# Kernel tuning notes

Measured on AMD Instinct MI355X. Metric: run time of the kernel, lower is better.

The kernel has to match this reference:

```python
import jax, jax.numpy as jnp
import numpy as np
from jax import lax

Z_DIM = 64
ZS_SIZE = [[1, 1]] * 12 + [[2, 1]] + [[2, 2]] * 11 + [[4, 2]] + [[4, 4]] * 11  # 36 embeddings
FILTER = [[16, 16]] * 6 + [[16, 32]] + [[32, 32]] * 5 + [[32, 64]] + [[64, 64]] * 5  # 18 blocks
OFFS = np.cumsum([0] + [h * k for h, k in ZS_SIZE]).tolist()  # 242 z-vectors total


def _hyper(Z, hn_w2, hn_b2, hn_w1, hn_b1):
    # Batched HyperNetwork: Z [n, 64] -> kernels [n, 16, 16, 3, 3]
    n = Z.shape[0]
    h_in = (Z @ hn_w2 + hn_b2).reshape(n, 16, Z_DIM)            # [n, 16, 64]
    h_fin = jnp.einsum('nid,do->nio', h_in, hn_w1) + hn_b1       # [n, 16, 144]
    return h_fin.reshape(n, 16, 16, 3, 3)


def _make_w(z_all, idx, hn_w2, hn_b2, hn_w1, hn_b1):
    # Assemble conv weight [h*16, k*16, 3, 3] from h*k hypernet tiles (cat dim=1 over k, dim=0 over h)
    h, k = ZS_SIZE[idx]
    Z = z_all[OFFS[idx]:OFFS[idx] + h * k]
    K = _hyper(Z, hn_w2, hn_b2, hn_w1, hn_b1)                    # [h*k, 16, 16, 3, 3]
    K = K.reshape(h, k, 16, 16, 3, 3).transpose(0, 2, 1, 3, 4, 5)
    return K.reshape(h * 16, k * 16, 3, 3)


def _conv(x, w, stride, pad):
    return lax.conv_general_dilated(x, w, (stride, stride), [(pad, pad), (pad, pad)],
                                    dimension_numbers=('NCHW', 'OIHW', 'NCHW'))


def _bn(x, i, g, b, m, v):
    # eval-mode BatchNorm2d with running stats; params padded to 64 channels
    C = x.shape[1]
    gg = g[i, :C].reshape(1, C, 1, 1)
    bb = b[i, :C].reshape(1, C, 1, 1)
    mm = m[i, :C].reshape(1, C, 1, 1)
    vv = v[i, :C].reshape(1, C, 1, 1)
    return (x - mm) * (gg * lax.rsqrt(vv + 1e-5)) + bb


def setup_inputs() -> dict:
    key = jax.random.key(0)
    ks = jax.random.split(key, 16)
    B = 1024
    x = jax.random.normal(ks[0], (B, 3, 32, 32), jnp.float32)
    conv1_w = jax.random.normal(ks[1], (16, 3, 3, 3), jnp.float32) / np.float32(np.sqrt(27.0))
    conv1_b = jnp.zeros((16,), jnp.float32)
    n_bn = 37  # bn1 + 2 per block
    bn_gamma = jnp.ones((n_bn, 64), jnp.float32)
    bn_beta = jnp.zeros((n_bn, 64), jnp.float32)
    bn_mean = jnp.zeros((n_bn, 64), jnp.float32)
    bn_var = jnp.ones((n_bn, 64), jnp.float32)
    hn_w2 = jax.random.normal(ks[2], (Z_DIM, 16 * Z_DIM), jnp.float32) * 0.04
    hn_b2 = jax.random.normal(ks[3], (16 * Z_DIM,), jnp.float32) * 0.01
    hn_w1 = jax.random.normal(ks[4], (Z_DIM, 16 * 9), jnp.float32) * 0.04
    hn_b1 = jax.random.normal(ks[5], (16 * 9,), jnp.float32) * 0.01
    z_all = jax.random.normal(ks[6], (OFFS[-1], Z_DIM), jnp.float32)
    res_w6 = jax.random.normal(ks[7], (32, 16, 1, 1), jnp.float32) * 0.25
    res_b6 = jnp.zeros((32,), jnp.float32)
    res_w12 = jax.random.normal(ks[8], (64, 32, 1, 1), jnp.float32) * 0.18
    res_b12 = jnp.zeros((64,), jnp.float32)
    fin_w = jax.random.normal(ks[9], (10, 64), jnp.float32) * 0.1
    fin_b = jnp.zeros((10,), jnp.float32)
    return {"x": x, "conv1_w": conv1_w, "conv1_b": conv1_b,
            "bn_gamma": bn_gamma, "bn_beta": bn_beta, "bn_mean": bn_mean, "bn_var": bn_var,
            "hn_w2": hn_w2, "hn_b2": hn_b2, "hn_w1": hn_w1, "hn_b1": hn_b1,
            "z_all": z_all, "res_w6": res_w6, "res_b6": res_b6,
            "res_w12": res_w12, "res_b12": res_b12, "fin_w": fin_w, "fin_b": fin_b}


def reference(x, conv1_w, conv1_b, bn_gamma, bn_beta, bn_mean, bn_var,
              hn_w2, hn_b2, hn_w1, hn_b1, z_all,
              res_w6, res_b6, res_w12, res_b12, fin_w, fin_b):
    x = _conv(x, conv1_w, 1, 1) + conv1_b.reshape(1, -1, 1, 1)
    x = jax.nn.relu(_bn(x, 0, bn_gamma, bn_beta, bn_mean, bn_var))
    for i in range(18):
        w1 = _make_w(z_all, 2 * i, hn_w2, hn_b2, hn_w1, hn_b1)
        w2 = _make_w(z_all, 2 * i + 1, hn_w2, hn_b2, hn_w1, hn_b1)
        down = (i > 5 and i % 6 == 0)
        if down:
            rw, rb = (res_w6, res_b6) if i == 6 else (res_w12, res_b12)
            res = _conv(x, rw, 2, 0) + rb.reshape(1, -1, 1, 1)
            stride = 2
        else:
            res = x
            stride = 1
        out = jax.nn.relu(_bn(_conv(x, w1, stride, 1), 1 + 2 * i, bn_gamma, bn_beta, bn_mean, bn_var))
        out = _bn(_conv(out, w2, 1, 1), 2 + 2 * i, bn_gamma, bn_beta, bn_mean, bn_var)
        x = jax.nn.relu(out + res)
    x = x.mean(axis=(2, 3))  # AvgPool2d(8) on [B,64,8,8]
    return x @ fin_w.T + fin_b
```

## Files before the change

### kernel.cpp

```cpp
#include <hip/hip_runtime.h>
#include <hip/hip_bf16.h>


typedef __attribute__((ext_vector_type(8))) short bf16x8;
typedef __attribute__((ext_vector_type(4))) float f32x4;
typedef __attribute__((ext_vector_type(16))) float f32x16;
typedef unsigned short ushort_t;

#define OFFS_LIST {0,1,2,3,4,5,6,7,8,9,10,11,12,14,18,22,26,30,34,38,42,46,50,54,58,66,82,98,114,130,146,162,178,194,210,226,242}
#define K_LIST    {1,1,1,1,1,1,1,1,1,1,1,1,1,2,2,2,2,2,2,2,2,2,2,2,2,4,4,4,4,4,4,4,4,4,4,4}
#define H_LIST    {1,1,1,1,1,1,1,1,1,1,1,1,2,2,2,2,2,2,2,2,2,2,2,2,4,4,4,4,4,4,4,4,4,4,4,4}
#define WOFF_LIST {0,2304,4608,6912,9216,11520,13824,16128,18432,20736,23040,25344,27648,32256,41472,50688,59904,69120,78336,87552,96768,105984,115200,124416,133632,152064,188928,225792,262656,299520,336384,373248,410112,446976,483840,520704}
#define CIN_LIST  {16,16,16,16,16,16,16,16,16,16,16,16,16,32,32,32,32,32,32,32,32,32,32,32,32,64,64,64,64,64,64,64,64,64,64,64}
#define COUT_LIST {16,16,16,16,16,16,16,16,16,16,16,16,32,32,32,32,32,32,32,32,32,32,32,32,64,64,64,64,64,64,64,64,64,64,64,64}
#define WFOFF_LIST {0,7680,15360,23040,30720,38400,46080,53760,61440,69120,76800,84480,92160,107520,135168,165888,196608,227328,258048,288768,319488,350208,380928,411648,442368,503808,632832,755712,878592,1001472,1124352,1247232,1370112,1492992,1615872,1738752}

__constant__ int d_offs[37]  = OFFS_LIST;
__constant__ int d_k[36]     = K_LIST;
__constant__ int d_hh[36]    = H_LIST;
__constant__ int d_woff[36]  = WOFF_LIST;
__constant__ int d_cin[36]   = CIN_LIST;
__constant__ int d_cout[36]  = COUT_LIST;
__constant__ int d_wfoff[36] = WFOFF_LIST;

__device__ inline void split3(float x, ushort_t& h, ushort_t& m, ushort_t& l) {
    unsigned xb = __float_as_uint(x);
    unsigned hb = (xb + 0x8000u) >> 16;
    float fh = __uint_as_float(hb << 16);
    float r = x - fh;
    unsigned mb = (__float_as_uint(r) + 0x8000u) >> 16;
    float fm = __uint_as_float(mb << 16);
    float r2 = r - fm;
    unsigned lb = (__float_as_uint(r2) + 0x8000u) >> 16;
    h = (ushort_t)hb; m = (ushort_t)mb; l = (ushort_t)lb;
}

__global__ void prep(const float* __restrict__ g, const float* __restrict__ be,
                     const float* __restrict__ m, const float* __restrict__ v,
                     const float* __restrict__ rw6, const float* __restrict__ rb12,
                     float* __restrict__ sc, float* __restrict__ sh,
                     float* __restrict__ rwT6, float* __restrict__ shp25) {
    int i = blockIdx.x * blockDim.x + threadIdx.x;
    if (i < 2368) {
        float s = g[i] * rsqrtf(v[i] + 1e-5f);
        sc[i] = s;
        sh[i] = be[i] - m[i] * s;
    } else if (i < 2368 + 512) {
        int t = i - 2368;
        int co = t % 32, ci = t / 32;
        rwT6[ci * 32 + co] = rw6[co * 16 + ci];
    } else if (i < 2368 + 512 + 64) {
        int c = i - 2880;
        int idx2 = 26 * 64 + c;
        float s = g[idx2] * rsqrtf(v[idx2] + 1e-5f);
        shp25[c] = be[idx2] - m[idx2] * s + rb12[c];
    }
}

__global__ void hyper_kernel(const float* __restrict__ z_all, const float* __restrict__ w2,
                             const float* __restrict__ b2, const float* __restrict__ w1,
                             const float* __restrict__ b1, const float* __restrict__ bnsc,
                             float* __restrict__ Wg) {
    int n = blockIdx.x;
    int tid = threadIdx.x;
    __shared__ float zrow[64];
    __shared__ float hin[1024];
    if (tid < 64) zrow[tid] = z_all[n * 64 + tid];
    __syncthreads();
    for (int mcol = tid; mcol < 1024; mcol += 256) {
        float acc = b2[mcol];
        #pragma unroll 8
        for (int d = 0; d < 64; ++d) acc += zrow[d] * w2[d * 1024 + mcol];
        hin[mcol] = acc;
    }
    __syncthreads();
    int L = 0;
    while (n >= d_offs[L + 1]) ++L;
    int r = n - d_offs[L];
    int kk = d_k[L];
    int a = r / kk, bb = r % kk;
    int Cin = kk * 16;
    int Cout = d_hh[L] * 16;
    const float* scp = bnsc + (L + 1) * 64;
    float* wp = Wg + d_woff[L];
    for (int e = tid; e < 2304; e += 256) {
        int i = e / 144, o = e % 144;
        int j = o / 9, tap = o % 9;
        float acc = b1[o];
        #pragma unroll 8
        for (int d = 0; d < 64; ++d) acc += hin[i * 64 + d] * w1[d * 144 + o];
        int co = a * 16 + i;
        acc *= scp[co];
        wp[(tap * Cin + (bb * 16 + j)) * Cout + co] = acc;
    }
}

__global__ void split_w(const float* __restrict__ Wg, const float* __restrict__ rw12,
                        ushort_t* __restrict__ Wf) {
    int L = blockIdx.y;
    int CIN = d_cin[L], COUT = d_cout[L];
    int idx = blockIdx.x * 256 + threadIdx.x;
    int j = idx & 7, lane = (idx >> 3) & 63, t = idx >> 9;
    int hi = lane >> 5;
    float wv;
    int base;
    if (L < 14) {
        int K = 9 * CIN, NKS = (K + 31) / 32, NT = COUT / 16;
        if (t >= NKS * NT) return;
        int nt = t % NT, ks = t / NT;
        int k = ks * 32 + (lane >> 4) * 8 + j;
        int co = nt * 16 + (lane & 15);
        wv = (k < K) ? Wg[d_woff[L] + k * COUT + co] : 0.f;
        base = d_wfoff[L] + ((ks * NT + nt) * 3) * 512 + lane * 8 + j;
    } else {
        int CG8 = CIN / 8, NKS = 5 * CG8, NT = COUT / 32;
        int TKS = NKS + ((L == 25) ? 2 : 0);
        if (t >= TKS * NT) return;
        int nt = t % NT, ks = t / NT;
        int co = nt * 32 + (lane & 31);
        if (ks < NKS) {
            int o = 2 * ks + hi, tap = o % 10, c8 = o / 10;
            int ci = c8 * 8 + j;
            wv = (tap < 9) ? Wg[d_woff[L] + (tap * CIN + ci) * COUT + co] : 0.f;
        } else {
            int k = (ks - NKS) * 16 + hi * 8 + j;
            wv = rw12[co * 32 + k];
        }
        base = d_wfoff[L] + ((ks * NT + nt) * 3) * 512 + lane * 8 + j;
    }
    ushort_t h, m, l;
    split3(wv, h, m, l);
    Wf[base] = h; Wf[base + 512] = m; Wf[base + 1024] = l;
}

__global__ void conv_first(const float* __restrict__ x, const float* __restrict__ cw,
                           const float* __restrict__ cb, const float* __restrict__ g,
                           const float* __restrict__ be, const float* __restrict__ m,
                           const float* __restrict__ v, float* __restrict__ out) {
    int idx = blockIdx.x * 256 + threadIdx.x;
    int px = idx & 31; int t = idx >> 5;
    int py = t & 31;   int b = t >> 5;
    float acc[16];
    #pragma unroll
    for (int co = 0; co < 16; ++co) acc[co] = 0.f;
    const float* ip = x + (long)b * 3 * 1024;
    #pragma unroll 1
    for (int ci = 0; ci < 3; ++ci) {
        #pragma unroll 1
        for (int ky = 0; ky < 3; ++ky) {
            int iy = py + ky - 1;
            if ((unsigned)iy >= 32u) continue;
            #pragma unroll
            for (int kx = 0; kx < 3; ++kx) {
                int ix = px + kx - 1;
                if ((unsigned)ix < 32u) {
                    float xv = ip[ci * 1024 + iy * 32 + ix];
                    #pragma unroll
                    for (int co = 0; co < 16; ++co)
                        acc[co] += xv * cw[co * 27 + ci * 9 + ky * 3 + kx];
                }
            }
        }
    }
    long o = ((long)(b * 32 + py) * 32 + px) * 16;
    #pragma unroll
    for (int co = 0; co < 16; ++co) {
        float s = g[co] * rsqrtf(v[co] + 1e-5f);
        float val = (acc[co] + cb[co] - m[co]) * s + be[co];
        out[o + co] = fmaxf(val, 0.f);
    }
}

__global__ void pad_zero_f32(float* __restrict__ buf, int H2, int C4) {
    int idx = blockIdx.x * 256 + threadIdx.x;
    int nb = 2 * H2 + 2 * (H2 - 2);
    int total = 1024 * nb * C4;
    if (idx >= total) return;
    int ch = idx % C4; int t = idx / C4;
    int bp = t % nb; int img = t / nb;
    int y, x;
    if (bp < H2) { y = 0; x = bp; }
    else if (bp < 2 * H2) { y = H2 - 1; x = bp - H2; }
    else { int s = bp - 2 * H2; y = 1 + (s >> 1); x = (s & 1) ? H2 - 1 : 0; }
    long off = (((long)img * H2 + y) * H2 + x) * (C4 * 4) + ch * 4;
    *(float4*)(buf + off) = make_float4(0.f, 0.f, 0.f, 0.f);
}

template<int MODE>
__global__ __launch_bounds__(256) void conv_s1(
        const float* __restrict__ in, const ushort_t* __restrict__ wf,
        const float* __restrict__ shp, const float* __restrict__ res,
        float* __restrict__ out) {
    constexpr int W2 = 34, SLABPIX = 10 * W2;
    constexpr int NKS = 5;

    __shared__ uint4 lds[6 * SLABPIX];

    int tid = threadIdx.x, lane = tid & 63, wid = tid >> 6;
    int g = lane >> 4, r16 = lane & 15;
    int bid = blockIdx.x;
    int img = bid >> 2, blocky = bid & 3;
    int row0 = blocky * 8;

    const ushort_t* wfl = wf + lane * 8;
    bf16x8 wv[NKS][3];
    #pragma unroll
    for (int ks = 0; ks < NKS; ++ks)
        #pragma unroll
        for (int p = 0; p < 3; ++p)
            wv[ks][p] = *(const bf16x8*)(wfl + (ks * 3 + p) * 512);
    #pragma unroll
    for (int ks = 0; ks < NKS; ++ks)
        #pragma unroll
        for (int p = 0; p < 3; ++p)
            asm volatile("" : "+v"(wv[ks][p]));

    const float* ib = in + (long)img * (32 * 32 * 16);
    for (int it = tid; it < SLABPIX * 2; it += 256) {
        int pix = it % SLABPIX, cc = it / SLABPIX;
        int sr = pix / W2, sc = pix % W2;
        int gy = row0 - 1 + sr, gx = sc - 1;
        float vv[8];
        if ((unsigned)gy < 32u && (unsigned)gx < 32u) {
            const float4* p4 = (const float4*)(ib + ((long)gy * 32 + gx) * 16 + cc * 8);
            float4 a0 = p4[0], a1 = p4[1];
            vv[0]=a0.x; vv[1]=a0.y; vv[2]=a0.z; vv[3]=a0.w;
            vv[4]=a1.x; vv[5]=a1.y; vv[6]=a1.z; vv[7]=a1.w;
        } else {
            #pragma unroll
            for (int q = 0; q < 8; ++q) vv[q] = 0.f;
        }
        union { ushort_t u[8]; uint4 q; } H, M, L;
        #pragma unroll
        for (int q = 0; q < 8; ++q) split3(vv[q], H.u[q], M.u[q], L.u[q]);
        lds[(cc * 3 + 0) * SLABPIX + pix] = H.q;
        lds[(cc * 3 + 1) * SLABPIX + pix] = M.q;
        lds[(cc * 3 + 2) * SLABPIX + pix] = L.q;
    }
    __syncthreads();

    int pbase[4];
    #pragma unroll
    for (int mt = 0; mt < 4; ++mt) {
        int pid = (wid * 4 + mt) * 16 + r16;
        pbase[mt] = (pid >> 5) * W2 + (pid & 31);
    }

    f32x4 acc[4] = {};

    #pragma unroll
    for (int ks = 0; ks < NKS; ++ks) {
        int k0 = ks * 32 + g * 8;
        int tap = k0 >> 4;
        int ci8 = (k0 >> 3) & 1;
        int ky = (tap * 11) >> 5;
        int kx = tap - 3 * ky;
        bool dead = (ks == NKS - 1) && (g >= 2);
        int ofs = dead ? 0 : (ci8 * 3) * SLABPIX + ky * W2 + kx;
        #pragma unroll
        for (int mt = 0; mt < 4; ++mt) {
            int e16 = dead ? 0 : ofs + pbase[mt];
            bf16x8 ah = *(const bf16x8*)&lds[e16];
            bf16x8 am = *(const bf16x8*)&lds[e16 + SLABPIX];
            bf16x8 al = *(const bf16x8*)&lds[e16 + 2 * SLABPIX];
            f32x4 c = acc[mt];
            c = __builtin_amdgcn_mfma_f32_16x16x32_bf16(ah, wv[ks][0], c, 0, 0, 0);
            c = __builtin_amdgcn_mfma_f32_16x16x32_bf16(ah, wv[ks][1], c, 0, 0, 0);
            c = __builtin_amdgcn_mfma_f32_16x16x32_bf16(am, wv[ks][0], c, 0, 0, 0);
            c = __builtin_amdgcn_mfma_f32_16x16x32_bf16(ah, wv[ks][2], c, 0, 0, 0);
            c = __builtin_amdgcn_mfma_f32_16x16x32_bf16(am, wv[ks][1], c, 0, 0, 0);
            c = __builtin_amdgcn_mfma_f32_16x16x32_bf16(al, wv[ks][0], c, 0, 0, 0);
            acc[mt] = c;
        }
    }

    #pragma unroll
    for (int mt = 0; mt < 4; ++mt) {
        #pragma unroll
        for (int reg = 0; reg < 4; ++reg) {
            int pid = (wid * 4 + mt) * 16 + g * 4 + reg;
            int gy = row0 + (pid >> 5), gx = pid & 31;
            long oidx = (((long)img * 32 + gy) * 32 + gx) * 16 + r16;
            float val = acc[mt][reg] + shp[r16];
            if (MODE == 1) val += res[oidx];
            out[oidx] = fmaxf(val, 0.f);
        }
    }
}

template<int CIN, int COUT, int HIN, int STRIDE, int TH, int TW, int MODE, int CR, int HR, int OUTF>
__global__ __launch_bounds__(256) void conv_mfma(
        const float* __restrict__ in, const ushort_t* __restrict__ wf,
        const float* __restrict__ shp, const float* __restrict__ res,
        const float* __restrict__ rwT, const float* __restrict__ rb,
        float* __restrict__ out) {
    constexpr int HOUT = HIN / STRIDE;
    constexpr int H2O = HOUT + 2;
    constexpr int CG8 = CIN / 8;
    constexpr int IH = (TH - 1) * STRIDE + 3;
    constexpr int IW = (TW - 1) * STRIDE + 3;
    constexpr int K = 9 * CIN;
    constexpr int NKS = (K + 31) / 32;
    constexpr bool TAIL = (K % 32) != 0;
    constexpr int NT = COUT / 16;
    constexpr int NMT = TH * TW / 16;
    constexpr int MTW = NMT / 4;
    constexpr int PADC = ((2 - (IH * IW)) % 8 + 8) % 8;
    constexpr int CSTU = IH * IW + PADC;
    constexpr int PST = CG8 * CSTU;
    constexpr int TX = HOUT / TW, TY = HOUT / TH;

    __shared__ uint4 lds[3 * PST];

    int tid = threadIdx.x;
    int bid = blockIdx.x;
    int tile = bid % (TY * TX);
    int b = bid / (TY * TX);
    int ty = tile / TX, tx = tile % TX;
    int Y0 = ty * TH, X0 = tx * TW;
    int gy0 = Y0 * STRIDE - 1, gx0 = X0 * STRIDE - 1;

    for (int e = tid; e < CG8 * IH * IW; e += 256) {
        int c8 = e / (IH * IW); int rr = e % (IH * IW);
        int ly = rr / IW, lx = rr % IW;
        int gy = gy0 + ly, gx = gx0 + lx;
        float vv[8];
        if ((unsigned)gy < (unsigned)HIN && (unsigned)gx < (unsigned)HIN) {
            const float4* p = (const float4*)(in + ((long)(b * HIN + gy) * HIN + gx) * CIN + c8 * 8);
            float4 a0 = p[0], a1 = p[1];
            vv[0]=a0.x; vv[1]=a0.y; vv[2]=a0.z; vv[3]=a0.w;
            vv[4]=a1.x; vv[5]=a1.y; vv[6]=a1.z; vv[7]=a1.w;
        } else {
            #pragma unroll
            for (int q = 0; q < 8; ++q) vv[q] = 0.f;
        }
        union { ushort_t u[8]; uint4 q4; } H, M, L;
        #pragma unroll
        for (int q = 0; q < 8; ++q) split3(vv[q], H.u[q], M.u[q], L.u[q]);
        int a16 = c8 * CSTU + rr;
        lds[a16] = H.q4; lds[PST + a16] = M.q4; lds[2 * PST + a16] = L.q4;
    }
    __syncthreads();

    int lane = tid & 63, wid = tid >> 6;
    int g = lane >> 4, r16 = lane & 15;

    f32x4 acc[MTW][NT] = {};

    int pbase[MTW];
    #pragma unroll
    for (int mt = 0; mt < MTW; ++mt) {
        int pid = (wid + 4 * mt) * 16 + r16;
        int py = pid / TW, px = pid % TW;
        pbase[mt] = (py * STRIDE) * IW + px * STRIDE;
    }

    #pragma unroll
    for (int ks = 0; ks < NKS; ++ks) {
        bf16x8 bfr[NT][3];
        #pragma unroll
        for (int nt = 0; nt < NT; ++nt)
            #pragma unroll
            for (int p = 0; p < 3; ++p)
                bfr[nt][p] = *(const bf16x8*)(wf + ((ks * NT + nt) * 3 + p) * 512 + lane * 8);

        int k0 = ks * 32 + g * 8;
        int tap = k0 / CIN;
        int ci8 = (k0 % CIN) >> 3;
        int ky = (tap * 11) >> 5;
        int kx = tap - 3 * ky;
        int ofs = ci8 * CSTU + ky * IW + kx;

        #pragma unroll
        for (int mt = 0; mt < MTW; ++mt) {
            int e16 = ofs + pbase[mt];
            if (TAIL && ks == NKS - 1) e16 = (g < 2) ? e16 : 0;
            const uint4* ap = lds + e16;
            bf16x8 ah = *(const bf16x8*)(ap);
            bf16x8 am = *(const bf16x8*)(ap + PST);
            bf16x8 al = *(const bf16x8*)(ap + 2 * PST);
            #pragma unroll
            for (int nt = 0; nt < NT; ++nt) {
                f32x4 c = acc[mt][nt];
                c = __builtin_amdgcn_mfma_f32_16x16x32_bf16(ah, bfr[nt][0], c, 0, 0, 0);
                c = __builtin_amdgcn_mfma_f32_16x16x32_bf16(ah, bfr[nt][1], c, 0, 0, 0);
                c = __builtin_amdgcn_mfma_f32_16x16x32_bf16(am, bfr[nt][0], c, 0, 0, 0);
                c = __builtin_amdgcn_mfma_f32_16x16x32_bf16(ah, bfr[nt][2], c, 0, 0, 0);
                c = __builtin_amdgcn_mfma_f32_16x16x32_bf16(am, bfr[nt][1], c, 0, 0, 0);
                c = __builtin_amdgcn_mfma_f32_16x16x32_bf16(al, bfr[nt][0], c, 0, 0, 0);
                acc[mt][nt] = c;
            }
        }
    }

    #pragma unroll
    for (int mt = 0; mt < MTW; ++mt) {
        #pragma unroll
        for (int nt = 0; nt < NT; ++nt) {
            int co = nt * 16 + r16;
            float shv = shp[co];
            #pragma unroll
            for (int reg = 0; reg < 4; ++reg) {
                int pid = (wid + 4 * mt) * 16 + g * 4 + reg;
                int py = pid / TW, px = pid % TW;
                int gy = Y0 + py, gx = X0 + px;
                float val = acc[mt][nt][reg] + shv;
                if (MODE == 1) {
                    long oidx = ((long)(b * HOUT + gy) * HOUT + gx) * COUT + co;
                    val += res[oidx];
                }
                if (MODE == 2) {
                    float racc = rb[co];
                    const float* rp = res + ((long)(b * HR + 2 * gy) * HR + 2 * gx) * CR;
                    #pragma unroll 4
                    for (int ci = 0; ci < CR; ++ci) racc += rp[ci] * rwT[ci * COUT + co];
                    val += racc;
                }
                val = fmaxf(val, 0.f);
                if (OUTF == 0) {
                    long oidx = ((long)(b * HOUT + gy) * HOUT + gx) * COUT + co;
                    out[oidx] = val;
                } else {
                    out[(((long)b * H2O + gy + 1) * H2O + gx + 1) * COUT + co] = val;
                }
            }
        }
    }
}

template<int CIN, int COUT, int HIN, int STRIDE, int PXB, int MODE, int RKS, int CHUNK>
__global__ __launch_bounds__(256) void conv_s23(
        const float* __restrict__ in, const ushort_t* __restrict__ wf,
        const float* __restrict__ shp, const float* __restrict__ res,
        float* __restrict__ out) {
    constexpr int HOUT = HIN / STRIDE;
    constexpr int H2I = HIN + 2, H2O = HOUT + 2;
    constexpr int C8 = CIN / 8;
    constexpr int NKS = 5 * C8;
    constexpr int TKS = NKS + RKS;
    constexpr int NC = TKS / CHUNK;
    constexpr int NTT = COUT / 32;
    constexpr int ROWSB = PXB / HOUT;
    constexpr int SLABR = (ROWSB - 1) * STRIDE + 3;
    constexpr int SLABPIX = SLABR * H2I;
    constexpr int NBLK = HOUT / ROWSB;
    constexpr int RESU = 3 * C8 * SLABPIX;
    constexpr int LDSU = RESU + ((MODE == 2) ? 12 * 64 : 0);

    __shared__ uint4 lds[LDSU];

    int tid = threadIdx.x, lane = tid & 63, wid = tid >> 6;
    int lp = lane & 31, hi = lane >> 5;
    int bid = blockIdx.x;
    int img = bid / NBLK, blocky = bid % NBLK;
    int pxg = wid / NTT, ntb = wid % NTT;
    int pix0 = pxg * 32 + lp;
    int py_blk = pix0 / HOUT, px = pix0 % HOUT;
    int py = blocky * ROWSB + py_blk;
    int slabrow0 = blocky * ROWSB * STRIDE;

    const ushort_t* wfl = wf + lane * 8;

    bf16x8 wA[CHUNK][3], wB[CHUNK][3];
    auto LW = [&](int c, bf16x8 (&w)[CHUNK][3]) {
        #pragma unroll
        for (int i = 0; i < CHUNK; ++i) {
            int ks = c * CHUNK + i;
            #pragma unroll
            for (int pp = 0; pp < 3; ++pp)
                w[i][pp] = *(const bf16x8*)(wfl + ((ks * NTT + ntb) * 3 + pp) * 512);
        }
    };

    LW(0, wA);
    if (NC > 1) LW(1, wB);

    const float* ib = in + (long)img * H2I * H2I * CIN;
    for (int it = tid; it < SLABPIX * C8; it += 256) {
        int pix = it % SLABPIX, cc = it / SLABPIX;
        int sr = pix / H2I, sc = pix % H2I;
        const float* p4 = ib + ((long)(slabrow0 + sr) * H2I + sc) * CIN + cc * 8;
        float4 a0 = ((const float4*)p4)[0], a1 = ((const float4*)p4)[1];
        float vv[8] = {a0.x, a0.y, a0.z, a0.w, a1.x, a1.y, a1.z, a1.w};
        union { ushort_t u[8]; uint4 q; } H, M, L;
        #pragma unroll
        for (int q = 0; q < 8; ++q) split3(vv[q], H.u[q], M.u[q], L.u[q]);
        int u0 = cc * 3;
        lds[u0 * SLABPIX + pix] = H.q;
        lds[(u0 + 1) * SLABPIX + pix] = M.q;
        lds[(u0 + 2) * SLABPIX + pix] = L.q;
    }
    if (MODE == 2) {
        for (int it = tid; it < 256; it += 256) {
            int pix = it & 63, cc = it >> 6;
            int ry = pix >> 3, rx = pix & 7;
            const float* r4 = res + (((long)img * 18 + (2 * ry + 1)) * 18 + (2 * rx + 1)) * 32 + cc * 8;
            float4 a0 = ((const float4*)r4)[0], a1 = ((const float4*)r4)[1];
            float vv[8] = {a0.x, a0.y, a0.z, a0.w, a1.x, a1.y, a1.z, a1.w};
            union { ushort_t u[8]; uint4 q; } H, M, L;
            #pragma unroll
            for (int q = 0; q < 8; ++q) split3(vv[q], H.u[q], M.u[q], L.u[q]);
            int u0 = RESU + cc * 3 * 64;
            lds[u0 + pix] = H.q;
            lds[u0 + 64 + pix] = M.q;
            lds[u0 + 128 + pix] = L.q;
        }
    }
    __syncthreads();

    int pbase = (py_blk * STRIDE) * H2I + px * STRIDE;
    f32x16 acc = {};

    auto DOC = [&](int c, bf16x8 (&w)[CHUNK][3]) {
        #pragma unroll
        for (int i = 0; i < CHUNK; ++i) {
            int ks = c * CHUNK + i;
            bf16x8 x0, x1, x2;
            if (RKS > 0 && ks >= NKS) {
                int o2 = 2 * (ks - NKS) + hi;
                int a = RESU + o2 * 3 * 64 + pix0;
                x0 = *(const bf16x8*)&lds[a];
                x1 = *(const bf16x8*)&lds[a + 64];
                x2 = *(const bf16x8*)&lds[a + 128];
            } else {
                int o = 2 * ks + hi;
                int tap = o % 10, c8i = o / 10;
                int ky = (tap * 11) >> 5, kx = tap - 3 * ky;
                int t16 = (tap == 9) ? 0 : (ky * H2I + kx);
                int a = (c8i * 3) * SLABPIX + pbase + t16;
                x0 = *(const bf16x8*)&lds[a];
                x1 = *(const bf16x8*)&lds[a + SLABPIX];
                x2 = *(const bf16x8*)&lds[a + 2 * SLABPIX];
            }
            acc = __builtin_amdgcn_mfma_f32_32x32x16_bf16(w[i][0], x0, acc, 0, 0, 0);
            acc = __builtin_amdgcn_mfma_f32_32x32x16_bf16(w[i][1], x0, acc, 0, 0, 0);
            acc = __builtin_amdgcn_mfma_f32_32x32x16_bf16(w[i][0], x1, acc, 0, 0, 0);
            acc = __builtin_amdgcn_mfma_f32_32x32x16_bf16(w[i][2], x0, acc, 0, 0, 0);
            acc = __builtin_amdgcn_mfma_f32_32x32x16_bf16(w[i][1], x1, acc, 0, 0, 0);
            acc = __builtin_amdgcn_mfma_f32_32x32x16_bf16(w[i][0], x2, acc, 0, 0, 0);
        }
    };

    #pragma unroll 1
    for (int c = 0; c < NC; c += 2) {
        DOC(c, wA);
        if (c + 2 < NC) LW(c + 2, wA);
        if (c + 1 < NC) DOC(c + 1, wB);
        if (c + 3 < NC) LW(c + 3, wB);
    }

    float* ob = out + (((long)img * H2O + py + 1) * H2O + (px + 1)) * COUT;
    const float* rb4 = (MODE == 1)
        ? res + (((long)img * H2O + py + 1) * H2O + (px + 1)) * COUT : nullptr;
    #pragma unroll
    for (int g = 0; g < 4; ++g) {
        int co = ntb * 32 + g * 8 + 4 * hi;
        float v0 = acc[4 * g + 0] + shp[co + 0];
        float v1 = acc[4 * g + 1] + shp[co + 1];
        float v2 = acc[4 * g + 2] + shp[co + 2];
        float v3 = acc[4 * g + 3] + shp[co + 3];
        if (MODE == 1) {
            float4 r = *(const float4*)(rb4 + co);
            v0 += r.x; v1 += r.y; v2 += r.z; v3 += r.w;
        }
        *(float4*)(ob + co) = make_float4(fmaxf(v0, 0.f), fmaxf(v1, 0.f),
                                          fmaxf(v2, 0.f), fmaxf(v3, 0.f));
    }
}

__global__ void pool_fc(const float* __restrict__ X, const float* __restrict__ fw,
                        const float* __restrict__ fb, float* __restrict__ out) {
    int b = blockIdx.x;
    int c = threadIdx.x;
    float s = 0.f;
    #pragma unroll
    for (int p = 0; p < 64; ++p) {
        int y = p >> 3, x = p & 7;
        s += X[(((long)b * 10 + y + 1) * 10 + (x + 1)) * 64 + c];
    }
    __shared__ float pooled[64];
    pooled[c] = s * (1.f / 64.f);
    __syncthreads();
    if (c < 10) {
        float acc = fb[c];
        #pragma unroll
        for (int k = 0; k < 64; ++k) acc += pooled[k] * fw[c * 64 + k];
        out[b * 10 + c] = acc;
    }
}

extern "C" void kernel_launch(void* const* d_in, const int* in_sizes, int n_in,
                              void* d_out, int out_size, void* d_ws, size_t ws_size,
                              hipStream_t stream) {
    const float* x       = (const float*)d_in[0];
    const float* conv1_w = (const float*)d_in[1];
    const float* conv1_b = (const float*)d_in[2];
    const float* bn_g    = (const float*)d_in[3];
    const float* bn_b    = (const float*)d_in[4];
    const float* bn_m    = (const float*)d_in[5];
    const float* bn_v    = (const float*)d_in[6];
    const float* hn_w2   = (const float*)d_in[7];
    const float* hn_b2   = (const float*)d_in[8];
    const float* hn_w1   = (const float*)d_in[9];
    const float* hn_b1   = (const float*)d_in[10];
    const float* z_all   = (const float*)d_in[11];
    const float* res_w6  = (const float*)d_in[12];
    const float* res_b6  = (const float*)d_in[13];
    const float* res_w12 = (const float*)d_in[14];
    const float* res_b12 = (const float*)d_in[15];
    const float* fin_w   = (const float*)d_in[16];
    const float* fin_b   = (const float*)d_in[17];
    float* outp = (float*)d_out;

    float* wsf      = (float*)d_ws;
    float* Wg       = wsf;
    float* bnsc     = wsf + 557568;
    float* bnsh     = wsf + 559936;
    float* rwT6     = wsf + 562304;
    float* shp25    = wsf + 564864;
    ushort_t* Wfrag = (ushort_t*)(wsf + 565248);

    float* A0f = (float*)((char*)d_ws + (size_t)(16) * (1 << 20));
    float* A1f = (float*)((char*)d_ws + (size_t)(80) * (1 << 20));
    float* A2f = (float*)((char*)d_ws + (size_t)(144) * (1 << 20));

    static const int wfoff[36] = WFOFF_LIST;

    prep<<<20, 256, 0, stream>>>(bn_g, bn_b, bn_m, bn_v, res_w6, res_b12,
                                 bnsc, bnsh, rwT6, shp25);
    hyper_kernel<<<242, 256, 0, stream>>>(z_all, hn_w2, hn_b2, hn_w1, hn_b1, bnsc, Wg);
    split_w<<<dim3(168, 36), 256, 0, stream>>>(Wg, res_w12, Wfrag);
    conv_first<<<4096, 256, 0, stream>>>(x, conv1_w, conv1_b, bn_g, bn_b, bn_m, bn_v, A0f);

    float* X = A0f; float* T1 = A1f; float* T2 = A2f;
    for (int i = 0; i < 6; ++i) {
        int L1 = 2 * i, L2 = 2 * i + 1;
        conv_s1<0><<<4096, 256, 0, stream>>>(
            X, Wfrag + wfoff[L1], bnsh + (L1 + 1) * 64, nullptr, T1);
        conv_s1<1><<<4096, 256, 0, stream>>>(
            T1, Wfrag + wfoff[L2], bnsh + (L2 + 1) * 64, X, T2);
        float* tmp = X; X = T2; T2 = tmp;
    }
    conv_mfma<16,32,32,2,8,16,0,1,1,0><<<2048, 256, 0, stream>>>(
        A0f, Wfrag + wfoff[12], bnsh + 13 * 64, nullptr, nullptr, nullptr, A1f);
    pad_zero_f32<<<2176, 256, 0, stream>>>(A2f, 18, 8);
    conv_mfma<32,32,16,1,8,16,2,16,32,2><<<2048, 256, 0, stream>>>(
        A1f, Wfrag + wfoff[13], bnsh + 14 * 64, A0f, rwT6, res_b6, A2f);
    pad_zero_f32<<<2176, 256, 0, stream>>>(A1f, 18, 8);
    pad_zero_f32<<<2176, 256, 0, stream>>>(A0f, 18, 8);

    X = A2f; T1 = A1f; T2 = A0f;
    for (int i = 7; i < 12; ++i) {
        int L1 = 2 * i, L2 = 2 * i + 1;
        conv_s23<32,32,16,1,128,0,0,5><<<2048, 256, 0, stream>>>(
            X, Wfrag + wfoff[L1], bnsh + (L1 + 1) * 64, nullptr, T1);
        conv_s23<32,32,16,1,128,1,0,5><<<2048, 256, 0, stream>>>(
            T1, Wfrag + wfoff[L2], bnsh + (L2 + 1) * 64, X, T2);
        float* tmp = X; X = T2; T2 = tmp;
    }
    pad_zero_f32<<<2304, 256, 0, stream>>>(A1f, 10, 16);
    conv_s23<32,64,16,2,64,0,0,5><<<1024, 256, 0, stream>>>(
        A0f, Wfrag + wfoff[24], bnsh + 25 * 64, nullptr, A1f);
    pad_zero_f32<<<2304, 256, 0, stream>>>(A2f, 10, 16);
    conv_s23<64,64,8,1,64,2,2,6><<<1024, 256, 0, stream>>>(
        A1f, Wfrag + wfoff[25], shp25, A0f, A2f);
    pad_zero_f32<<<2304, 256, 0, stream>>>(A0f, 10, 16);

    X = A2f; T1 = A1f; T2 = A0f;
    for (int i = 13; i < 18; ++i) {
        int L1 = 2 * i, L2 = 2 * i + 1;
        conv_s23<64,64,8,1,64,0,0,5><<<1024, 256, 0, stream>>>(
            X, Wfrag + wfoff[L1], bnsh + (L1 + 1) * 64, nullptr, T1);
        conv_s23<64,64,8,1,64,1,0,5><<<1024, 256, 0, stream>>>(
            T1, Wfrag + wfoff[L2], bnsh + (L2 + 1) * 64, X, T2);
        float* tmp = X; X = T2; T2 = tmp;
    }
    pool_fc<<<1024, 64, 0, stream>>>(A0f, fin_w, fin_b, outp);
}
```

Before: 1.477 ms.

## Fuse residual block conv pairs into one kernel with LDS-resident intermediate

Adds a block_fused kernel that runs both 3x3 convs of a residual block per image, keeping the split-bf16 intermediate activation and the residual input in LDS instead of writing and re-reading it through global memory. It also folds the stride-2 1x1 projection shortcut of block 6 into the MFMA K-loop as extra weight slices, as was already done for block 12, and removes the scalar residual-add paths. This cuts kernel launches and global activation traffic for stages 2 and 3. In exchange, each workgroup is one image with a large LDS footprint, which may lower occupancy, and the buffer rotation and padding logic are rearranged.

```diff
diff --git a/kernel.cpp b/kernel.cpp
--- a/kernel.cpp
+++ b/kernel.cpp
@@ -13,7 +13,7 @@
 #define WOFF_LIST {0,2304,4608,6912,9216,11520,13824,16128,18432,20736,23040,25344,27648,32256,41472,50688,59904,69120,78336,87552,96768,105984,115200,124416,133632,152064,188928,225792,262656,299520,336384,373248,410112,446976,483840,520704}
 #define CIN_LIST  {16,16,16,16,16,16,16,16,16,16,16,16,16,32,32,32,32,32,32,32,32,32,32,32,32,64,64,64,64,64,64,64,64,64,64,64}
 #define COUT_LIST {16,16,16,16,16,16,16,16,16,16,16,16,32,32,32,32,32,32,32,32,32,32,32,32,64,64,64,64,64,64,64,64,64,64,64,64}
-#define WFOFF_LIST {0,7680,15360,23040,30720,38400,46080,53760,61440,69120,76800,84480,92160,107520,135168,165888,196608,227328,258048,288768,319488,350208,380928,411648,442368,503808,632832,755712,878592,1001472,1124352,1247232,1370112,1492992,1615872,1738752}
+#define WFOFF_LIST {0,7680,15360,23040,30720,38400,46080,53760,61440,69120,76800,84480,92160,107520,139776,170496,201216,231936,262656,293376,324096,354816,385536,416256,446976,508416,637440,760320,883200,1006080,1128960,1251840,1374720,1497600,1620480,1743360}
 
 __constant__ int d_offs[37]  = OFFS_LIST;
 __constant__ int d_k[36]     = K_LIST;
@@ -34,23 +34,25 @@
     unsigned lb = (__float_as_uint(r2) + 0x8000u) >> 16;
     h = (ushort_t)hb; m = (ushort_t)mb; l = (ushort_t)lb;
 }
+__device__ inline float b2f(ushort_t u) { return __uint_as_float(((unsigned)u) << 16); }
 
 __global__ void prep(const float* __restrict__ g, const float* __restrict__ be,
                      const float* __restrict__ m, const float* __restrict__ v,
-                     const float* __restrict__ rw6, const float* __restrict__ rb12,
+                     const float* __restrict__ rb6, const float* __restrict__ rb12,
                      float* __restrict__ sc, float* __restrict__ sh,
-                     float* __restrict__ rwT6, float* __restrict__ shp25) {
+                     float* __restrict__ shp13, float* __restrict__ shp25) {
     int i = blockIdx.x * blockDim.x + threadIdx.x;
     if (i < 2368) {
         float s = g[i] * rsqrtf(v[i] + 1e-5f);
         sc[i] = s;
         sh[i] = be[i] - m[i] * s;
-    } else if (i < 2368 + 512) {
-        int t = i - 2368;
-        int co = t % 32, ci = t / 32;
-        rwT6[ci * 32 + co] = rw6[co * 16 + ci];
-    } else if (i < 2368 + 512 + 64) {
-        int c = i - 2880;
+    } else if (i < 2368 + 32) {
+        int c = i - 2368;
+        int idx2 = 14 * 64 + c;
+        float s = g[idx2] * rsqrtf(v[idx2] + 1e-5f);
+        shp13[c] = be[idx2] - m[idx2] * s + rb6[c];
+    } else if (i < 2400 + 64) {
+        int c = i - 2400;
         int idx2 = 26 * 64 + c;
         float s = g[idx2] * rsqrtf(v[idx2] + 1e-5f);
         shp25[c] = be[idx2] - m[idx2] * s + rb12[c];
@@ -95,8 +97,8 @@
     }
 }
 
-__global__ void split_w(const float* __restrict__ Wg, const float* __restrict__ rw12,
-                        ushort_t* __restrict__ Wf) {
+__global__ void split_w(const float* __restrict__ Wg, const float* __restrict__ rw6,
+                        const float* __restrict__ rw12, ushort_t* __restrict__ Wf) {
     int L = blockIdx.y;
     int CIN = d_cin[L], COUT = d_cout[L];
     int idx = blockIdx.x * 256 + threadIdx.x;
@@ -104,7 +106,7 @@
     int hi = lane >> 5;
     float wv;
     int base;
-    if (L < 14) {
+    if (L < 13) {
         int K = 9 * CIN, NKS = (K + 31) / 32, NT = COUT / 16;
         if (t >= NKS * NT) return;
         int nt = t % NT, ks = t / NT;
@@ -114,7 +116,7 @@
         base = d_wfoff[L] + ((ks * NT + nt) * 3) * 512 + lane * 8 + j;
     } else {
         int CG8 = CIN / 8, NKS = 5 * CG8, NT = COUT / 32;
-        int TKS = NKS + ((L == 25) ? 2 : 0);
+        int TKS = NKS + ((L == 25) ? 2 : ((L == 13) ? 1 : 0));
         if (t >= TKS * NT) return;
         int nt = t % NT, ks = t / NT;
         int co = nt * 32 + (lane & 31);
@@ -122,9 +124,12 @@
             int o = 2 * ks + hi, tap = o % 10, c8 = o / 10;
             int ci = c8 * 8 + j;
             wv = (tap < 9) ? Wg[d_woff[L] + (tap * CIN + ci) * COUT + co] : 0.f;
-        } else {
+        } else if (L == 25) {
             int k = (ks - NKS) * 16 + hi * 8 + j;
             wv = rw12[co * 32 + k];
+        } else {
+            int k = hi * 8 + j;
+            wv = rw6[co * 16 + k];
         }
         base = d_wfoff[L] + ((ks * NT + nt) * 3) * 512 + lane * 8 + j;
     }
@@ -288,12 +293,10 @@
     }
 }
 
-template<int CIN, int COUT, int HIN, int STRIDE, int TH, int TW, int MODE, int CR, int HR, int OUTF>
+template<int CIN, int COUT, int HIN, int STRIDE, int TH, int TW, int OUTF>
 __global__ __launch_bounds__(256) void conv_mfma(
         const float* __restrict__ in, const ushort_t* __restrict__ wf,
-        const float* __restrict__ shp, const float* __restrict__ res,
-        const float* __restrict__ rwT, const float* __restrict__ rb,
-        float* __restrict__ out) {
+        const float* __restrict__ shp, float* __restrict__ out) {
     constexpr int HOUT = HIN / STRIDE;
     constexpr int H2O = HOUT + 2;
     constexpr int CG8 = CIN / 8;
@@ -303,8 +306,7 @@
     constexpr int NKS = (K + 31) / 32;
     constexpr bool TAIL = (K % 32) != 0;
     constexpr int NT = COUT / 16;
-    constexpr int NMT = TH * TW / 16;
-    constexpr int MTW = NMT / 4;
+    constexpr int MTW = TH * TW / 64;
     constexpr int PADC = ((2 - (IH * IW)) % 8 + 8) % 8;
     constexpr int CSTU = IH * IW + PADC;
     constexpr int PST = CG8 * CSTU;
@@ -404,22 +406,9 @@
                 int pid = (wid + 4 * mt) * 16 + g * 4 + reg;
                 int py = pid / TW, px = pid % TW;
                 int gy = Y0 + py, gx = X0 + px;
-                float val = acc[mt][nt][reg] + shv;
-                if (MODE == 1) {
-                    long oidx = ((long)(b * HOUT + gy) * HOUT + gx) * COUT + co;
-                    val += res[oidx];
-                }
-                if (MODE == 2) {
-                    float racc = rb[co];
-                    const float* rp = res + ((long)(b * HR + 2 * gy) * HR + 2 * gx) * CR;
-                    #pragma unroll 4
-                    for (int ci = 0; ci < CR; ++ci) racc += rp[ci] * rwT[ci * COUT + co];
-                    val += racc;
-                }
-                val = fmaxf(val, 0.f);
+                float val = fmaxf(acc[mt][nt][reg] + shv, 0.f);
                 if (OUTF == 0) {
-                    long oidx = ((long)(b * HOUT + gy) * HOUT + gx) * COUT + co;
-                    out[oidx] = val;
+                    out[((long)(b * HOUT + gy) * HOUT + gx) * COUT + co] = val;
                 } else {
                     out[(((long)b * H2O + gy + 1) * H2O + gx + 1) * COUT + co] = val;
                 }
@@ -445,7 +434,7 @@
     constexpr int SLABPIX = SLABR * H2I;
     constexpr int NBLK = HOUT / ROWSB;
     constexpr int RESU = 3 * C8 * SLABPIX;
-    constexpr int LDSU = RESU + ((MODE == 2) ? 12 * 64 : 0);
+    constexpr int LDSU = RESU + ((MODE == 2) ? 768 : ((MODE == 3) ? 768 : 0));
 
     __shared__ uint4 lds[LDSU];
 
@@ -506,6 +495,23 @@
             lds[u0 + 128 + pix] = L.q;
         }
     }
+    if (MODE == 3) {
+        for (int it = tid; it < 256; it += 256) {
+            int opix = it >> 1, cg = it & 1;
+            int r = opix / 16, cxx = opix % 16;
+            int gy = (blocky * 8 + r) * 2, gx = cxx * 2;
+            const float* r4 = res + (((long)img * 32 + gy) * 32 + gx) * 16 + cg * 8;
+            float4 a0 = ((const float4*)r4)[0], a1 = ((const float4*)r4)[1];
+            float vv[8] = {a0.x, a0.y, a0.z, a0.w, a1.x, a1.y, a1.z, a1.w};
+            union { ushort_t u[8]; uint4 q; } H, M, L;
+            #pragma unroll
+            for (int q = 0; q < 8; ++q) split3(vv[q], H.u[q], M.u[q], L.u[q]);
+            int u0 = RESU + opix * 6;
+            lds[u0 + cg] = H.q;
+            lds[u0 + 2 + cg] = M.q;
+            lds[u0 + 4 + cg] = L.q;
+        }
+    }
     __syncthreads();
 
     int pbase = (py_blk * STRIDE) * H2I + px * STRIDE;
@@ -517,11 +523,18 @@
             int ks = c * CHUNK + i;
             bf16x8 x0, x1, x2;
             if (RKS > 0 && ks >= NKS) {
-                int o2 = 2 * (ks - NKS) + hi;
-                int a = RESU + o2 * 3 * 64 + pix0;
-                x0 = *(const bf16x8*)&lds[a];
-                x1 = *(const bf16x8*)&lds[a + 64];
-                x2 = *(const bf16x8*)&lds[a + 128];
+                if (MODE == 2) {
+                    int o2 = 2 * (ks - NKS) + hi;
+                    int a = RESU + o2 * 3 * 64 + pix0;
+                    x0 = *(const bf16x8*)&lds[a];
+                    x1 = *(const bf16x8*)&lds[a + 64];
+                    x2 = *(const bf16x8*)&lds[a + 128];
+                } else {
+                    int a = RESU + pix0 * 6 + hi;
+                    x0 = *(const bf16x8*)&lds[a];
+                    x1 = *(const bf16x8*)&lds[a + 2];
+                    x2 = *(const bf16x8*)&lds[a + 4];
+                }
             } else {
                 int o = 2 * ks + hi;
                 int tap = o % 10, c8i = o / 10;
@@ -545,13 +558,10 @@
     for (int c = 0; c < NC; c += 2) {
         DOC(c, wA);
         if (c + 2 < NC) LW(c + 2, wA);
-        if (c + 1 < NC) DOC(c + 1, wB);
-        if (c + 3 < NC) LW(c + 3, wB);
+        if (c + 1 < NC) { DOC(c + 1, wB); if (c + 3 < NC) LW(c + 3, wB); }
     }
 
     float* ob = out + (((long)img * H2O + py + 1) * H2O + (px + 1)) * COUT;
-    const float* rb4 = (MODE == 1)
-        ? res + (((long)img * H2O + py + 1) * H2O + (px + 1)) * COUT : nullptr;
     #pragma unroll
     for (int g = 0; g < 4; ++g) {
         int co = ntb * 32 + g * 8 + 4 * hi;
@@ -559,12 +569,163 @@
         float v1 = acc[4 * g + 1] + shp[co + 1];
         float v2 = acc[4 * g + 2] + shp[co + 2];
         float v3 = acc[4 * g + 3] + shp[co + 3];
-        if (MODE == 1) {
-            float4 r = *(const float4*)(rb4 + co);
-            v0 += r.x; v1 += r.y; v2 += r.z; v3 += r.w;
-        }
         *(float4*)(ob + co) = make_float4(fmaxf(v0, 0.f), fmaxf(v1, 0.f),
                                           fmaxf(v2, 0.f), fmaxf(v3, 0.f));
+    }
+}
+
+template<int CIN, int HIN, int TPW>
+__global__ __launch_bounds__(256) void block_fused(
+        const float* __restrict__ in, const ushort_t* __restrict__ wf1,
+        const ushort_t* __restrict__ wf2, const float* __restrict__ sh1,
+        const float* __restrict__ sh2, float* __restrict__ out) {
+    constexpr int H2 = HIN + 2, H2PIX = H2 * H2;
+    constexpr int C8 = CIN / 8;
+    constexpr int NKS = 5 * C8;
+    constexpr int CHUNK = 5, NC = NKS / CHUNK;
+    constexpr int NTT = CIN / 32;
+    constexpr int BUFU = 3 * C8 * H2PIX;
+
+    __shared__ uint4 lds[2 * BUFU];
+    ushort_t* lsh = (ushort_t*)lds;
+
+    int tid = threadIdx.x, lane = tid & 63, wid = tid >> 6;
+    int lp = lane & 31, hi = lane >> 5;
+    int img = blockIdx.x;
+
+    int ntb0 = (wid * TPW) % NTT;
+    int pb[TPW];
+    #pragma unroll
+    for (int t = 0; t < TPW; ++t) {
+        int tl = wid * TPW + t;
+        int pix = (tl / NTT) * 32 + lp;
+        pb[t] = (pix / HIN + 1) * H2 + (pix % HIN + 1);
+    }
+
+    const float* ib = in + (long)img * H2PIX * CIN;
+    for (int it = tid; it < H2PIX * C8; it += 256) {
+        int cc = it % C8, pix = it / C8;
+        const float4* p4 = (const float4*)(ib + (long)pix * CIN + cc * 8);
+        float4 a0 = p4[0], a1 = p4[1];
+        float vv[8] = {a0.x, a0.y, a0.z, a0.w, a1.x, a1.y, a1.z, a1.w};
+        union { ushort_t u[8]; uint4 q; } H, M, L;
+        #pragma unroll
+        for (int q = 0; q < 8; ++q) split3(vv[q], H.u[q], M.u[q], L.u[q]);
+        lds[(cc * 3 + 0) * H2PIX + pix] = H.q;
+        lds[(cc * 3 + 1) * H2PIX + pix] = M.q;
+        lds[(cc * 3 + 2) * H2PIX + pix] = L.q;
+    }
+    constexpr int NB = 4 * H2 - 4;
+    uint4 zq = make_uint4(0, 0, 0, 0);
+    for (int it = tid; it < NB * C8; it += 256) {
+        int bp = it % NB, cc = it / NB;
+        int y, x;
+        if (bp < H2) { y = 0; x = bp; }
+        else if (bp < 2 * H2) { y = H2 - 1; x = bp - H2; }
+        else { int s = bp - 2 * H2; y = 1 + (s >> 1); x = (s & 1) ? H2 - 1 : 0; }
+        int pix = y * H2 + x;
+        lds[BUFU + (cc * 3 + 0) * H2PIX + pix] = zq;
+        lds[BUFU + (cc * 3 + 1) * H2PIX + pix] = zq;
+        lds[BUFU + (cc * 3 + 2) * H2PIX + pix] = zq;
+    }
+    __syncthreads();
+
+    bf16x8 wA[CHUNK][3], wB[CHUNK][3];
+    f32x16 acc[TPW];
+
+    auto CONV = [&](int bb, const ushort_t* wf) {
+        const ushort_t* wfl = wf + lane * 8;
+        #pragma unroll
+        for (int t = 0; t < TPW; ++t)
+            #pragma unroll
+            for (int q = 0; q < 16; ++q) acc[t][q] = 0.f;
+        auto LW = [&](int c, bf16x8 (&w)[CHUNK][3]) {
+            #pragma unroll
+            for (int i = 0; i < CHUNK; ++i) {
+                int ks = c * CHUNK + i;
+                #pragma unroll
+                for (int pp = 0; pp < 3; ++pp)
+                    w[i][pp] = *(const bf16x8*)(wfl + ((ks * NTT + ntb0) * 3 + pp) * 512);
+            }
+        };
+        auto DOC = [&](int c, bf16x8 (&w)[CHUNK][3]) {
+            #pragma unroll
+            for (int i = 0; i < CHUNK; ++i) {
+                int ks = c * CHUNK + i;
+                int o = 2 * ks + hi;
+                int tap = o % 10, c8i = o / 10;
+                int ky = (tap * 11) >> 5, kx = tap - 3 * ky;
+                int rel = (tap == 9) ? 0 : (ky - 1) * H2 + (kx - 1);
+                #pragma unroll
+                for (int t = 0; t < TPW; ++t) {
+                    int a = (tap == 9) ? (c8i * 3) * H2PIX
+                                       : (c8i * 3) * H2PIX + pb[t] + rel;
+                    bf16x8 x0 = *(const bf16x8*)&lds[bb + a];
+                    bf16x8 x1 = *(const bf16x8*)&lds[bb + a + H2PIX];
+                    bf16x8 x2 = *(const bf16x8*)&lds[bb + a + 2 * H2PIX];
+                    f32x16 c2 = acc[t];
+                    c2 = __builtin_amdgcn_mfma_f32_32x32x16_bf16(w[i][0], x0, c2, 0, 0, 0);
+                    c2 = __builtin_amdgcn_mfma_f32_32x32x16_bf16(w[i][1], x0, c2, 0, 0, 0);
+                    c2 = __builtin_amdgcn_mfma_f32_32x32x16_bf16(w[i][0], x1, c2, 0, 0, 0);
+                    c2 = __builtin_amdgcn_mfma_f32_32x32x16_bf16(w[i][2], x0, c2, 0, 0, 0);
+                    c2 = __builtin_amdgcn_mfma_f32_32x32x16_bf16(w[i][1], x1, c2, 0, 0, 0);
+                    c2 = __builtin_amdgcn_mfma_f32_32x32x16_bf16(w[i][0], x2, c2, 0, 0, 0);
+                    acc[t] = c2;
+                }
+            }
+        };
+        LW(0, wA);
+        if (NC > 1) LW(1, wB);
+        #pragma unroll 1
+        for (int c = 0; c < NC; c += 2) {
+            DOC(c, wA);
+            if (c + 2 < NC) LW(c + 2, wA);
+            if (c + 1 < NC) { DOC(c + 1, wB); if (c + 3 < NC) LW(c + 3, wB); }
+        }
+    };
+
+    CONV(0, wf1);
+    #pragma unroll
+    for (int t = 0; t < TPW; ++t) {
+        #pragma unroll
+        for (int q = 0; q < 4; ++q) {
+            int co = ntb0 * 32 + q * 8 + 4 * hi;
+            int c8o = co >> 3;
+            ushort4 h4, m4, l4;
+            #pragma unroll
+            for (int e = 0; e < 4; ++e) {
+                float val = fmaxf(acc[t][4 * q + e] + sh1[co + e], 0.f);
+                ushort_t h, m2, l;
+                split3(val, h, m2, l);
+                ((ushort_t*)&h4)[e] = h; ((ushort_t*)&m4)[e] = m2; ((ushort_t*)&l4)[e] = l;
+            }
+            int so = ((BUFU + (c8o * 3) * H2PIX + pb[t]) << 3) + (co & 7);
+            *(ushort4*)&lsh[so] = h4;
+            *(ushort4*)&lsh[so + H2PIX * 8] = m4;
+            *(ushort4*)&lsh[so + 2 * H2PIX * 8] = l4;
+        }
+    }
+    __syncthreads();
+
+    CONV(BUFU, wf2);
+    float* ob = out + (long)img * H2PIX * CIN;
+    #pragma unroll
+    for (int t = 0; t < TPW; ++t) {
+        #pragma unroll
+        for (int q = 0; q < 4; ++q) {
+            int co = ntb0 * 32 + q * 8 + 4 * hi;
+            int c8o = co >> 3;
+            int so = (((c8o * 3) * H2PIX + pb[t]) << 3) + (co & 7);
+            ushort4 rh = *(const ushort4*)&lsh[so];
+            ushort4 rm = *(const ushort4*)&lsh[so + H2PIX * 8];
+            ushort4 rl = *(const ushort4*)&lsh[so + 2 * H2PIX * 8];
+            float v0 = acc[t][4 * q + 0] + sh2[co + 0] + b2f(rh.x) + b2f(rm.x) + b2f(rl.x);
+            float v1 = acc[t][4 * q + 1] + sh2[co + 1] + b2f(rh.y) + b2f(rm.y) + b2f(rl.y);
+            float v2 = acc[t][4 * q + 2] + sh2[co + 2] + b2f(rh.z) + b2f(rm.z) + b2f(rl.z);
+            float v3 = acc[t][4 * q + 3] + sh2[co + 3] + b2f(rh.w) + b2f(rm.w) + b2f(rl.w);
+            *(float4*)(ob + (long)pb[t] * CIN + co) =
+                make_float4(fmaxf(v0, 0.f), fmaxf(v1, 0.f), fmaxf(v2, 0.f), fmaxf(v3, 0.f));
+        }
     }
 }
 
@@ -616,7 +777,7 @@
     float* Wg       = wsf;
     float* bnsc     = wsf + 557568;
     float* bnsh     = wsf + 559936;
-    float* rwT6     = wsf + 562304;
+    float* shp13    = wsf + 562304;
     float* shp25    = wsf + 564864;
     ushort_t* Wfrag = (ushort_t*)(wsf + 565248);
 
@@ -626,10 +787,10 @@
 
     static const int wfoff[36] = WFOFF_LIST;
 
-    prep<<<20, 256, 0, stream>>>(bn_g, bn_b, bn_m, bn_v, res_w6, res_b12,
-                                 bnsc, bnsh, rwT6, shp25);
+    prep<<<20, 256, 0, stream>>>(bn_g, bn_b, bn_m, bn_v, res_b6, res_b12,
+                                 bnsc, bnsh, shp13, shp25);
     hyper_kernel<<<242, 256, 0, stream>>>(z_all, hn_w2, hn_b2, hn_w1, hn_b1, bnsc, Wg);
-    split_w<<<dim3(168, 36), 256, 0, stream>>>(Wg, res_w12, Wfrag);
+    split_w<<<dim3(168, 36), 256, 0, stream>>>(Wg, res_w6, res_w12, Wfrag);
     conv_first<<<4096, 256, 0, stream>>>(x, conv1_w, conv1_b, bn_g, bn_b, bn_m, bn_v, A0f);
 
     float* X = A0f; float* T1 = A1f; float* T2 = A2f;
@@ -641,39 +802,35 @@
             T1, Wfrag + wfoff[L2], bnsh + (L2 + 1) * 64, X, T2);
         float* tmp = X; X = T2; T2 = tmp;
     }
-    conv_mfma<16,32,32,2,8,16,0,1,1,0><<<2048, 256, 0, stream>>>(
-        A0f, Wfrag + wfoff[12], bnsh + 13 * 64, nullptr, nullptr, nullptr, A1f);
+    pad_zero_f32<<<2176, 256, 0, stream>>>(A1f, 18, 8);
+    conv_mfma<16,32,32,2,8,16,1><<<2048, 256, 0, stream>>>(
+        A0f, Wfrag + wfoff[12], bnsh + 13 * 64, A1f);
     pad_zero_f32<<<2176, 256, 0, stream>>>(A2f, 18, 8);
-    conv_mfma<32,32,16,1,8,16,2,16,32,2><<<2048, 256, 0, stream>>>(
-        A1f, Wfrag + wfoff[13], bnsh + 14 * 64, A0f, rwT6, res_b6, A2f);
-    pad_zero_f32<<<2176, 256, 0, stream>>>(A1f, 18, 8);
-    pad_zero_f32<<<2176, 256, 0, stream>>>(A0f, 18, 8);
-
-    X = A2f; T1 = A1f; T2 = A0f;
+    conv_s23<32,32,16,1,128,3,1,3><<<2048, 256, 0, stream>>>(
+        A1f, Wfrag + wfoff[13], shp13, A0f, A2f);
+
+    X = A2f; T1 = A1f;
     for (int i = 7; i < 12; ++i) {
         int L1 = 2 * i, L2 = 2 * i + 1;
-        conv_s23<32,32,16,1,128,0,0,5><<<2048, 256, 0, stream>>>(
-            X, Wfrag + wfoff[L1], bnsh + (L1 + 1) * 64, nullptr, T1);
-        conv_s23<32,32,16,1,128,1,0,5><<<2048, 256, 0, stream>>>(
-            T1, Wfrag + wfoff[L2], bnsh + (L2 + 1) * 64, X, T2);
-        float* tmp = X; X = T2; T2 = tmp;
-    }
-    pad_zero_f32<<<2304, 256, 0, stream>>>(A1f, 10, 16);
+        block_fused<32,16,2><<<1024, 256, 0, stream>>>(
+            X, Wfrag + wfoff[L1], Wfrag + wfoff[L2],
+            bnsh + (L1 + 1) * 64, bnsh + (L2 + 1) * 64, T1);
+        float* tmp = X; X = T1; T1 = tmp;
+    }
+    pad_zero_f32<<<2304, 256, 0, stream>>>(A0f, 10, 16);
     conv_s23<32,64,16,2,64,0,0,5><<<1024, 256, 0, stream>>>(
-        A0f, Wfrag + wfoff[24], bnsh + 25 * 64, nullptr, A1f);
+        A1f, Wfrag + wfoff[24], bnsh + 25 * 64, nullptr, A0f);
     pad_zero_f32<<<2304, 256, 0, stream>>>(A2f, 10, 16);
     conv_s23<64,64,8,1,64,2,2,6><<<1024, 256, 0, stream>>>(
-        A1f, Wfrag + wfoff[25], shp25, A0f, A2f);
-    pad_zero_f32<<<2304, 256, 0, stream>>>(A0f, 10, 16);
-
-    X = A2f; T1 = A1f; T2 = A0f;
+        A0f, Wfrag + wfoff[25], shp25, A1f, A2f);
+
+    X = A2f; T1 = A0f;
     for (int i = 13; i < 18; ++i) {
         int L1 = 2 * i, L2 = 2 * i + 1;
-        conv_s23<64,64,8,1,64,0,0,5><<<1024, 256, 0, stream>>>(
-            X, Wfrag + wfoff[L1], bnsh + (L1 + 1) * 64, nullptr, T1);
-        conv_s23<64,64,8,1,64,1,0,5><<<1024, 256, 0, stream>>>(
-            T1, Wfrag + wfoff[L2], bnsh + (L2 + 1) * 64, X, T2);
-        float* tmp = X; X = T2; T2 = tmp;
+        block_fused<64,8,1><<<1024, 256, 0, stream>>>(
+            X, Wfrag + wfoff[L1], Wfrag + wfoff[L2],
+            bnsh + (L1 + 1) * 64, bnsh + (L2 + 1) * 64, T1);
+        float* tmp = X; X = T1; T1 = tmp;
     }
     pool_fc<<<1024, 64, 0, stream>>>(A0f, fin_w, fin_b, outp);
 }
```

Measured after the change: 1.368 ms. -7.4%, faster.
